# Kernel tuning notes

Hardware: AMD Instinct MI355X
Metric: run time of the kernel (lower is better)

Reference implementation:

```python
import jax, jax.numpy as jnp
import numpy as np

# priors from init_kwargs
PRIOR_PI = 0.5
PRIOR_S1 = 1.0
PRIOR_S2 = 0.0025
LOG_SQRT_2PI = 0.5 * np.log(2.0 * np.pi).astype(np.float32)


def _normal_logprob(x, sigma):
    # Normal(0, sigma).log_prob(x)
    return -0.5 * (x / sigma) ** 2 - jnp.log(sigma) - LOG_SQRT_2PI


def _mixture_logprob_sum(x, pi, sigma1, sigma2):
    # log(pi * N(x;0,s1) + (1-pi) * N(x;0,s2)).sum(), as in the torch code
    p1 = jnp.exp(_normal_logprob(x, sigma1))
    p2 = jnp.exp(_normal_logprob(x, sigma2))
    return jnp.log(pi * p1 + (1.0 - pi) * p2).sum()


def _sample(pi, rho1, rho2, eps, gum):
    # ScaleMixtureGaussian_VarPost.sample(): gumbel-max over (pi, 1-pi)
    sigma1 = jnp.log1p(jnp.exp(rho1))
    sigma2 = jnp.log1p(jnp.exp(rho2))
    x = jnp.stack((pi, 1.0 - pi), axis=-1)          # [..., 2]
    mode = jnp.argmax(x + gum, axis=-1).astype(pi.dtype)  # [...]
    return mode * sigma1 * eps + (1.0 - mode) * sigma2 * eps


def setup_inputs() -> dict:
    key = jax.random.key(0)
    ks = jax.random.split(key, 12)
    OUT, IN, B = 8192, 4096, 128
    f32 = jnp.float32
    u_w = jax.random.uniform(ks[0], (OUT, IN, 2), dtype=f32, minval=1e-6, maxval=1.0 - 1e-6)
    u_b = jax.random.uniform(ks[1], (OUT, 2), dtype=f32, minval=1e-6, maxval=1.0 - 1e-6)
    return {
        "x": jax.random.normal(ks[2], (B, IN), dtype=f32),
        "w_pi": jax.random.uniform(ks[3], (OUT, IN), dtype=f32),
        "w_rho1": 0.1 * jax.random.normal(ks[4], (OUT, IN), dtype=f32),
        "w_rho2": 0.1 * jax.random.normal(ks[5], (OUT, IN), dtype=f32),
        "b_pi": jax.random.uniform(ks[6], (OUT,), dtype=f32),
        "b_rho1": 0.1 * jax.random.normal(ks[7], (OUT,), dtype=f32),
        "b_rho2": 0.1 * jax.random.normal(ks[8], (OUT,), dtype=f32),
        "eps_w": jax.random.normal(ks[9], (OUT, IN), dtype=f32),
        "eps_b": jax.random.normal(ks[10], (OUT,), dtype=f32),
        "gum_w": -jnp.log(-jnp.log(u_w)),  # Gumbel(0,1)
        "gum_b": -jnp.log(-jnp.log(u_b)),
    }


def reference(x, w_pi, w_rho1, w_rho2, b_pi, b_rho1, b_rho2, eps_w, eps_b, gum_w, gum_b):
    weight = _sample(w_pi, w_rho1, w_rho2, eps_w, gum_w)   # [OUT, IN]
    bias = _sample(b_pi, b_rho1, b_rho2, eps_b, gum_b)     # [OUT]

    log_prior = (_mixture_logprob_sum(weight, PRIOR_PI, PRIOR_S1, PRIOR_S2)
                 + _mixture_logprob_sum(bias, PRIOR_PI, PRIOR_S1, PRIOR_S2))

    sig_w1 = jnp.log1p(jnp.exp(w_rho1))
    sig_w2 = jnp.log1p(jnp.exp(w_rho2))
    sig_b1 = jnp.log1p(jnp.exp(b_rho1))
    sig_b2 = jnp.log1p(jnp.exp(b_rho2))
    log_post = (_mixture_logprob_sum(weight, w_pi, sig_w1, sig_w2)
                + _mixture_logprob_sum(bias, b_pi, sig_b1, sig_b2))

    out = x @ weight.T + bias  # F.linear
    return out, log_prior, log_post
```

## Files before the change

kernel.cpp:

```cpp
#include <hip/hip_runtime.h>

#define OUTN 8192
#define INN  4096
#define BN   128

namespace {

typedef __attribute__((ext_vector_type(8))) short bf16x8;
typedef __attribute__((ext_vector_type(4))) float f32x4;

struct alignas(16) f4 { float v[4]; };
struct alignas(8)  h4 { short v[4]; };

constexpr float C_HLOG2PI = 0.91893853f;
constexpr float C_LN2     = 0.69314718f;

__device__ __forceinline__ short f2bf(float f) {
    unsigned u = __float_as_uint(f);
    u += 0x7fffu + ((u >> 16) & 1u);
    return (short)(u >> 16);
}

__device__ __forceinline__ float prior_lp(float w) {
    float lp1 = -0.5f * w * w - C_HLOG2PI;
    float a   = w * 400.0f;
    float lp2 = -0.5f * a * a + 5.0725261f;
    return __logf(0.5f * __expf(lp1) + 0.5f * __expf(lp2));
}
__device__ __forceinline__ float post_lp(float w, float pi_, float s1, float ls1,
                                         float s2, float ls2) {
    float u1  = __fdividef(w, s1);
    float u2  = __fdividef(w, s2);
    float lq1 = -0.5f * u1 * u1 - ls1 - C_HLOG2PI;
    float lq2 = -0.5f * u2 * u2 - ls2 - C_HLOG2PI;
    return __logf(pi_ * __expf(lq1) + (1.0f - pi_) * __expf(lq2));
}
__device__ __forceinline__ float sample_w(float pi_, float rho1, float rho2, float ep,
                                          float g0, float g1,
                                          float& s1, float& ls1, float& s2, float& ls2) {
    s1  = __logf(1.0f + __expf(rho1));
    s2  = __logf(1.0f + __expf(rho2));
    ls1 = __logf(s1);
    ls2 = __logf(s2);
    bool mode1 = ((1.0f - pi_) + g1) > (pi_ + g0);
    return (mode1 ? s1 : s2) * ep;
}

constexpr int OT = 32;
constexpr int KC = 32;
constexpr int NT = 256;
constexpr int KSTR = 40;

__global__ __launch_bounds__(256)
void xcast(const float* __restrict__ x, short* __restrict__ xb)
{
    const int i = (blockIdx.x * 256 + threadIdx.x) * 8;
    f4 a = *(const f4*)&x[i];
    f4 b = *(const f4*)&x[i + 4];
    h4 o0, o1;
    #pragma unroll
    for (int j = 0; j < 4; ++j) { o0.v[j] = f2bf(a.v[j]); o1.v[j] = f2bf(b.v[j]); }
    *(h4*)&xb[i]     = o0;
    *(h4*)&xb[i + 4] = o1;
}

__global__ __launch_bounds__(NT, 6)
void bayes_main(const short* __restrict__ xb,
                const float* __restrict__ w_pi,
                const float* __restrict__ w_rho1,
                const float* __restrict__ w_rho2,
                const float* __restrict__ eps_w,
                const float* __restrict__ gum_w,
                const float* __restrict__ bias,
                float* __restrict__ out,
                float* __restrict__ pbuf,
                float* __restrict__ partials,
                int NS)
{
    __shared__ alignas(16) short Wt[OT][KSTR];
    __shared__ alignas(16) short Xs[BN][KSTR];
    __shared__ float red[8];

    const int tid   = threadIdx.x;
    const int split = blockIdx.x >> 8;
    const int tile  = blockIdx.x & 255;
    const int o0    = tile * OT;

    const int baseCh = 128 / NS;
    const int remCh  = 128 % NS;
    const int nch    = baseCh + (split < remCh ? 1 : 0);
    const int ch0    = split * baseCh + (split < remCh ? split : remCh);
    const int k0     = ch0 * KC;

    float* outp = (split == 0) ? out : pbuf + (size_t)(split - 1) * ((size_t)BN * OUTN);

    const int c = tid & 7;
    const int r = tid >> 3;

    const size_t wbase = (size_t)(o0 + r) * INN + k0;
    const f4* pi4 = (const f4*)(w_pi   + wbase) + c;
    const f4* r14 = (const f4*)(w_rho1 + wbase) + c;
    const f4* r24 = (const f4*)(w_rho2 + wbase) + c;
    const f4* ep4 = (const f4*)(eps_w  + wbase) + c;
    const f4* gm4 = (const f4*)(gum_w  + 2 * wbase) + 2 * c;

    const int xrr = tid >> 1;
    const int xcc = (tid & 1) * 16;
    const short* xsrc = xb + (size_t)xrr * INN + k0 + xcc;

    f32x4 acc00 = {0.f,0.f,0.f,0.f}, acc01 = {0.f,0.f,0.f,0.f};
    f32x4 acc10 = {0.f,0.f,0.f,0.f}, acc11 = {0.f,0.f,0.f,0.f};
    float priorAcc = 0.0f, postAcc = 0.0f;

    const int wv_  = tid >> 6;
    const int lane = tid & 63;
    const int lrow = lane & 15;
    const int lgo  = (lane >> 4) * 8;

    f4 vpi = pi4[0], vr1 = r14[0], vr2 = r24[0], vep = ep4[0];
    f4 vga = gm4[0], vgb = gm4[1];
    bf16x8 xv0 = *(const bf16x8*)(xsrc);
    bf16x8 xv1 = *(const bf16x8*)(xsrc + 8);

    #pragma unroll 1
    for (int t = 0; t < nch; ++t) {
        h4 wb;
        #pragma unroll
        for (int i = 0; i < 4; ++i) {
            const f4& g = (i < 2) ? vga : vgb;
            float g0 = g.v[(i & 1) * 2], g1 = g.v[(i & 1) * 2 + 1];
            float pi_ = vpi.v[i], ep = vep.v[i];
            float s1  = __logf(1.0f + __expf(vr1.v[i]));
            float s2  = __logf(1.0f + __expf(vr2.v[i]));
            float ls1 = __logf(s1), ls2 = __logf(s2);
            bool  m1  = ((1.0f - pi_) + g1) > (pi_ + g0);
            float sm  = m1 ? s1 : s2;
            float so  = m1 ? s2 : s1;
            float lsm = m1 ? ls1 : ls2;
            float lso = m1 ? ls2 : ls1;
            float wm  = m1 ? pi_ : 1.0f - pi_;
            float w   = sm * ep;
            wb.v[i] = f2bf(w);
            float wsq = w * w;
            float dlp = 5.9914645f - 79999.5f * wsq;
            priorAcc += -0.5f * wsq + __logf(1.0f + __expf(dlp));
            float uo   = __fdividef(w, so);
            float epsq = ep * ep;
            float dlq  = 0.5f * (epsq - uo * uo) + (lsm - lso);
            postAcc += -0.5f * epsq - lsm
                       + __logf(wm + (1.0f - wm) * __expf(dlq));
        }

        __syncthreads();
        *(h4*)&Wt[r][4 * c] = wb;
        *(bf16x8*)&Xs[xrr][xcc]     = xv0;
        *(bf16x8*)&Xs[xrr][xcc + 8] = xv1;
        __syncthreads();

        const int tn = (t + 1 < nch) ? t + 1 : 0;
        vpi = pi4[8*tn]; vr1 = r14[8*tn]; vr2 = r24[8*tn]; vep = ep4[8*tn];
        vga = gm4[16*tn]; vgb = gm4[16*tn + 1];
        xv0 = *(const bf16x8*)(xsrc + 32*tn);
        xv1 = *(const bf16x8*)(xsrc + 32*tn + 8);

        bf16x8 a0 = *(const bf16x8*)&Xs[32 * wv_      + lrow][lgo];
        bf16x8 a1 = *(const bf16x8*)&Xs[32 * wv_ + 16 + lrow][lgo];
        bf16x8 b0 = *(const bf16x8*)&Wt[lrow     ][lgo];
        bf16x8 b1 = *(const bf16x8*)&Wt[16 + lrow][lgo];
        acc00 = __builtin_amdgcn_mfma_f32_16x16x32_bf16(a0, b0, acc00, 0, 0, 0);
        acc01 = __builtin_amdgcn_mfma_f32_16x16x32_bf16(a0, b1, acc01, 0, 0, 0);
        acc10 = __builtin_amdgcn_mfma_f32_16x16x32_bf16(a1, b0, acc10, 0, 0, 0);
        acc11 = __builtin_amdgcn_mfma_f32_16x16x32_bf16(a1, b1, acc11, 0, 0, 0);
    }

    {
        const float ne = (float)(4 * nch);
        priorAcc -= ne * (C_HLOG2PI + C_LN2);
        postAcc  -= ne * C_HLOG2PI;
    }

    {
        const int oc = o0 + lrow;
        const int bb = 32 * wv_ + (lane >> 4) * 4;
        const float bv0 = bias ? bias[oc]      : 0.0f;
        const float bv1 = bias ? bias[oc + 16] : 0.0f;
        #pragma unroll
        for (int j = 0; j < 4; ++j) {
            outp[(size_t)(bb      + j) * OUTN + oc     ] = acc00[j] + bv0;
            outp[(size_t)(bb      + j) * OUTN + oc + 16] = acc01[j] + bv1;
            outp[(size_t)(bb + 16 + j) * OUTN + oc     ] = acc10[j] + bv0;
            outp[(size_t)(bb + 16 + j) * OUTN + oc + 16] = acc11[j] + bv1;
        }
    }

    #pragma unroll
    for (int off = 32; off; off >>= 1) {
        priorAcc += __shfl_down(priorAcc, off);
        postAcc  += __shfl_down(postAcc, off);
    }
    if ((tid & 63) == 0) { red[wv_] = priorAcc; red[4 + wv_] = postAcc; }
    __syncthreads();
    if (tid == 0) {
        partials[2*blockIdx.x    ] = red[0] + red[1] + red[2] + red[3];
        partials[2*blockIdx.x + 1] = red[4] + red[5] + red[6] + red[7];
    }
}

__global__ __launch_bounds__(256)
void bayes_bias(const float* __restrict__ b_pi, const float* __restrict__ b_rho1,
                const float* __restrict__ b_rho2, const float* __restrict__ eps_b,
                const float* __restrict__ gum_b,
                float* __restrict__ bias_vals, float* __restrict__ bpart)
{
    __shared__ float red[8];
    const int tid = threadIdx.x;
    const int o = blockIdx.x * 256 + tid;
    float pi_ = b_pi[o], rho1 = b_rho1[o], rho2 = b_rho2[o], ep = eps_b[o];
    float g0 = gum_b[2*o], g1 = gum_b[2*o + 1];
    float s1, ls1, s2, ls2;
    float w = sample_w(pi_, rho1, rho2, ep, g0, g1, s1, ls1, s2, ls2);
    bias_vals[o] = w;
    float pa = prior_lp(w);
    float qa = post_lp(w, pi_, s1, ls1, s2, ls2);
    #pragma unroll
    for (int off = 32; off; off >>= 1) {
        pa += __shfl_down(pa, off);
        qa += __shfl_down(qa, off);
    }
    const int wave = tid >> 6;
    if ((tid & 63) == 0) { red[wave] = pa; red[4 + wave] = qa; }
    __syncthreads();
    if (tid == 0) {
        bpart[2*blockIdx.x    ] = red[0] + red[1] + red[2] + red[3];
        bpart[2*blockIdx.x + 1] = red[4] + red[5] + red[6] + red[7];
    }
}

__global__ __launch_bounds__(256)
void bayes_reduce(float* __restrict__ out, const float* __restrict__ pbuf,
                  const float* __restrict__ bias, int nsplit)
{
    const size_t i = ((size_t)blockIdx.x * 256 + threadIdx.x) * 4;
    const int o = (int)(i & (OUTN - 1));
    f4 a  = *(const f4*)&out[i];
    f4 bq = *(const f4*)&bias[o];
    #pragma unroll 1
    for (int s = 0; s < nsplit - 1; ++s) {
        f4 p = *(const f4*)&pbuf[(size_t)s * ((size_t)BN * OUTN) + i];
        #pragma unroll
        for (int j = 0; j < 4; ++j) a.v[j] += p.v[j];
    }
    #pragma unroll
    for (int j = 0; j < 4; ++j) a.v[j] += bq.v[j];
    *(f4*)&out[i] = a;
}

__global__ __launch_bounds__(256)
void bayes_final(const float* __restrict__ partials, int cnt,
                 float* __restrict__ out_scalars)
{
    __shared__ double sp[4], sq[4];
    const int tid = threadIdx.x;
    double p = 0.0, q = 0.0;
    for (int j = tid; j < cnt; j += 256) {
        p += (double)partials[2*j];
        q += (double)partials[2*j + 1];
    }
    #pragma unroll
    for (int off = 32; off; off >>= 1) {
        p += __shfl_down(p, off);
        q += __shfl_down(q, off);
    }
    const int wave = tid >> 6;
    if ((tid & 63) == 0) { sp[wave] = p; sq[wave] = q; }
    __syncthreads();
    if (tid == 0) {
        out_scalars[0] = (float)(sp[0] + sp[1] + sp[2] + sp[3]);
        out_scalars[1] = (float)(sq[0] + sq[1] + sq[2] + sq[3]);
    }
}

}

extern "C" void kernel_launch(void* const* d_in, const int* in_sizes, int n_in,
                              void* d_out, int out_size, void* d_ws, size_t ws_size,
                              hipStream_t stream) {
    (void)in_sizes; (void)n_in; (void)out_size;
    const float* x      = (const float*)d_in[0];
    const float* w_pi   = (const float*)d_in[1];
    const float* w_rho1 = (const float*)d_in[2];
    const float* w_rho2 = (const float*)d_in[3];
    const float* b_pi   = (const float*)d_in[4];
    const float* b_rho1 = (const float*)d_in[5];
    const float* b_rho2 = (const float*)d_in[6];
    const float* eps_w  = (const float*)d_in[7];
    const float* eps_b  = (const float*)d_in[8];
    const float* gum_w  = (const float*)d_in[9];
    const float* gum_b  = (const float*)d_in[10];

    float* out = (float*)d_out;
    float* ws  = (float*)d_ws;
    float* bias_vals = ws;
    float* partials  = ws + 8192;
    short* xb        = (short*)(ws + 16384);
    float* pbuf      = ws + 540672;

    const size_t outElems = (size_t)BN * OUTN;
    int NS = 1;
    if      (ws_size >= (540672 + 5 * outElems) * sizeof(float)) NS = 6;
    else if (ws_size >= (540672 + 3 * outElems) * sizeof(float)) NS = 4;
    else if (ws_size >= (540672 + 1 * outElems) * sizeof(float)) NS = 2;

    float* bpart = partials + 2 * 256 * NS;
    const int cnt = 256 * NS + 32;

    xcast<<<(BN * INN) / (256 * 8), 256, 0, stream>>>(x, xb);
    bayes_bias<<<32, 256, 0, stream>>>(b_pi, b_rho1, b_rho2, eps_b, gum_b,
                                       bias_vals, bpart);

    if (NS == 1) {
        bayes_main<<<256, NT, 0, stream>>>(xb, w_pi, w_rho1, w_rho2, eps_w, gum_w,
                                           bias_vals, out, pbuf, partials, 1);
    } else {
        bayes_main<<<256 * NS, NT, 0, stream>>>(xb, w_pi, w_rho1, w_rho2, eps_w, gum_w,
                                                nullptr, out, pbuf, partials, NS);
        bayes_reduce<<<(int)(outElems / 4 / 256), 256, 0, stream>>>(out, pbuf,
                                                                    bias_vals, NS);
    }
    bayes_final<<<1, 256, 0, stream>>>(partials, cnt, out + outElems);
}
```

Baseline: 201.5 us.

## Double-buffer LDS tiles in main loop and fuse auxiliary kernels

The main GEMM loop now uses two LDS buffers alternated per chunk, which replaces the two __syncthreads per iteration with a single waitcnt plus barrier. The next chunk's global loads are issued before the barrier. The x-cast and bias-sampling kernels are merged into one prep launch, and the split-K reduction is merged with the final scalar reduction, cutting two kernel launches. The cost is double the LDS per block, which may lower occupancy. The reduction in block 0 depends on every main-kernel partial being written, which stream order guarantees.

Result: slower. 223.6 us (+10.9%).

```diff
diff --git a/kernel.cpp b/kernel.cpp
--- a/kernel.cpp
+++ b/kernel.cpp
@@ -52,16 +52,46 @@
 constexpr int KSTR = 40;
 
 __global__ __launch_bounds__(256)
-void xcast(const float* __restrict__ x, short* __restrict__ xb)
+void prep(const float* __restrict__ x, short* __restrict__ xb,
+          const float* __restrict__ b_pi, const float* __restrict__ b_rho1,
+          const float* __restrict__ b_rho2, const float* __restrict__ eps_b,
+          const float* __restrict__ gum_b,
+          float* __restrict__ bias_vals, float* __restrict__ bpart)
 {
-    const int i = (blockIdx.x * 256 + threadIdx.x) * 8;
-    f4 a = *(const f4*)&x[i];
-    f4 b = *(const f4*)&x[i + 4];
-    h4 o0, o1;
+    __shared__ float red[8];
+    const int tid = threadIdx.x;
+    if (blockIdx.x < 256) {
+        const int i = (blockIdx.x * 256 + tid) * 8;
+        f4 a = *(const f4*)&x[i];
+        f4 b = *(const f4*)&x[i + 4];
+        h4 o0, o1;
+        #pragma unroll
+        for (int j = 0; j < 4; ++j) { o0.v[j] = f2bf(a.v[j]); o1.v[j] = f2bf(b.v[j]); }
+        *(h4*)&xb[i]     = o0;
+        *(h4*)&xb[i + 4] = o1;
+        return;
+    }
+    const int bb = blockIdx.x - 256;
+    const int o = bb * 256 + tid;
+    float pi_ = b_pi[o], rho1 = b_rho1[o], rho2 = b_rho2[o], ep = eps_b[o];
+    float g0 = gum_b[2*o], g1 = gum_b[2*o + 1];
+    float s1, ls1, s2, ls2;
+    float w = sample_w(pi_, rho1, rho2, ep, g0, g1, s1, ls1, s2, ls2);
+    bias_vals[o] = w;
+    float pa = prior_lp(w);
+    float qa = post_lp(w, pi_, s1, ls1, s2, ls2);
     #pragma unroll
-    for (int j = 0; j < 4; ++j) { o0.v[j] = f2bf(a.v[j]); o1.v[j] = f2bf(b.v[j]); }
-    *(h4*)&xb[i]     = o0;
-    *(h4*)&xb[i + 4] = o1;
+    for (int off = 32; off; off >>= 1) {
+        pa += __shfl_down(pa, off);
+        qa += __shfl_down(qa, off);
+    }
+    const int wave = tid >> 6;
+    if ((tid & 63) == 0) { red[wave] = pa; red[4 + wave] = qa; }
+    __syncthreads();
+    if (tid == 0) {
+        bpart[2*bb    ] = red[0] + red[1] + red[2] + red[3];
+        bpart[2*bb + 1] = red[4] + red[5] + red[6] + red[7];
+    }
 }
 
 __global__ __launch_bounds__(NT, 6)
@@ -77,8 +107,8 @@
                 float* __restrict__ partials,
                 int NS)
 {
-    __shared__ alignas(16) short Wt[OT][KSTR];
-    __shared__ alignas(16) short Xs[BN][KSTR];
+    __shared__ alignas(16) short Wt[2][OT][KSTR];
+    __shared__ alignas(16) short Xs[2][BN][KSTR];
     __shared__ float red[8];
 
     const int tid   = threadIdx.x;
@@ -124,6 +154,7 @@
 
     #pragma unroll 1
     for (int t = 0; t < nch; ++t) {
+        const int p = t & 1;
         h4 wb;
         #pragma unroll
         for (int i = 0; i < 4; ++i) {
@@ -151,22 +182,24 @@
                        + __logf(wm + (1.0f - wm) * __expf(dlq));
         }
 
-        __syncthreads();
-        *(h4*)&Wt[r][4 * c] = wb;
-        *(bf16x8*)&Xs[xrr][xcc]     = xv0;
-        *(bf16x8*)&Xs[xrr][xcc + 8] = xv1;
-        __syncthreads();
-
         const int tn = (t + 1 < nch) ? t + 1 : 0;
         vpi = pi4[8*tn]; vr1 = r14[8*tn]; vr2 = r24[8*tn]; vep = ep4[8*tn];
         vga = gm4[16*tn]; vgb = gm4[16*tn + 1];
+
+        *(h4*)&Wt[p][r][4 * c] = wb;
+        *(bf16x8*)&Xs[p][xrr][xcc]     = xv0;
+        *(bf16x8*)&Xs[p][xrr][xcc + 8] = xv1;
         xv0 = *(const bf16x8*)(xsrc + 32*tn);
         xv1 = *(const bf16x8*)(xsrc + 32*tn + 8);
 
-        bf16x8 a0 = *(const bf16x8*)&Xs[32 * wv_      + lrow][lgo];
-        bf16x8 a1 = *(const bf16x8*)&Xs[32 * wv_ + 16 + lrow][lgo];
-        bf16x8 b0 = *(const bf16x8*)&Wt[lrow     ][lgo];
-        bf16x8 b1 = *(const bf16x8*)&Wt[16 + lrow][lgo];
+        asm volatile("s_waitcnt lgkmcnt(0)" ::: "memory");
+        __builtin_amdgcn_s_barrier();
+        asm volatile("" ::: "memory");
+
+        bf16x8 a0 = *(const bf16x8*)&Xs[p][32 * wv_      + lrow][lgo];
+        bf16x8 a1 = *(const bf16x8*)&Xs[p][32 * wv_ + 16 + lrow][lgo];
+        bf16x8 b0 = *(const bf16x8*)&Wt[p][lrow     ][lgo];
+        bf16x8 b1 = *(const bf16x8*)&Wt[p][16 + lrow][lgo];
         acc00 = __builtin_amdgcn_mfma_f32_16x16x32_bf16(a0, b0, acc00, 0, 0, 0);
         acc01 = __builtin_amdgcn_mfma_f32_16x16x32_bf16(a0, b1, acc01, 0, 0, 0);
         acc10 = __builtin_amdgcn_mfma_f32_16x16x32_bf16(a1, b0, acc10, 0, 0, 0);
@@ -207,40 +240,13 @@
 }
 
 __global__ __launch_bounds__(256)
-void bayes_bias(const float* __restrict__ b_pi, const float* __restrict__ b_rho1,
-                const float* __restrict__ b_rho2, const float* __restrict__ eps_b,
-                const float* __restrict__ gum_b,
-                float* __restrict__ bias_vals, float* __restrict__ bpart)
+void reduce_final(float* __restrict__ out, const float* __restrict__ pbuf,
+                  const float* __restrict__ bias, int nsplit,
+                  const float* __restrict__ partials, int cnt,
+                  float* __restrict__ out_scalars)
 {
-    __shared__ float red[8];
     const int tid = threadIdx.x;
-    const int o = blockIdx.x * 256 + tid;
-    float pi_ = b_pi[o], rho1 = b_rho1[o], rho2 = b_rho2[o], ep = eps_b[o];
-    float g0 = gum_b[2*o], g1 = gum_b[2*o + 1];
-    float s1, ls1, s2, ls2;
-    float w = sample_w(pi_, rho1, rho2, ep, g0, g1, s1, ls1, s2, ls2);
-    bias_vals[o] = w;
-    float pa = prior_lp(w);
-    float qa = post_lp(w, pi_, s1, ls1, s2, ls2);
-    #pragma unroll
-    for (int off = 32; off; off >>= 1) {
-        pa += __shfl_down(pa, off);
-        qa += __shfl_down(qa, off);
-    }
-    const int wave = tid >> 6;
-    if ((tid & 63) == 0) { red[wave] = pa; red[4 + wave] = qa; }
-    __syncthreads();
-    if (tid == 0) {
-        bpart[2*blockIdx.x    ] = red[0] + red[1] + red[2] + red[3];
-        bpart[2*blockIdx.x + 1] = red[4] + red[5] + red[6] + red[7];
-    }
-}
-
-__global__ __launch_bounds__(256)
-void bayes_reduce(float* __restrict__ out, const float* __restrict__ pbuf,
-                  const float* __restrict__ bias, int nsplit)
-{
-    const size_t i = ((size_t)blockIdx.x * 256 + threadIdx.x) * 4;
+    const size_t i = ((size_t)blockIdx.x * 256 + tid) * 4;
     const int o = (int)(i & (OUTN - 1));
     f4 a  = *(const f4*)&out[i];
     f4 bq = *(const f4*)&bias[o];
@@ -253,6 +259,27 @@
     #pragma unroll
     for (int j = 0; j < 4; ++j) a.v[j] += bq.v[j];
     *(f4*)&out[i] = a;
+
+    if (blockIdx.x == 0) {
+        __shared__ double sp[4], sq[4];
+        double p = 0.0, q = 0.0;
+        for (int j = tid; j < cnt; j += 256) {
+            p += (double)partials[2*j];
+            q += (double)partials[2*j + 1];
+        }
+        #pragma unroll
+        for (int off = 32; off; off >>= 1) {
+            p += __shfl_down(p, off);
+            q += __shfl_down(q, off);
+        }
+        const int wave = tid >> 6;
+        if ((tid & 63) == 0) { sp[wave] = p; sq[wave] = q; }
+        __syncthreads();
+        if (tid == 0) {
+            out_scalars[0] = (float)(sp[0] + sp[1] + sp[2] + sp[3]);
+            out_scalars[1] = (float)(sq[0] + sq[1] + sq[2] + sq[3]);
+        }
+    }
 }
 
 __global__ __launch_bounds__(256)
@@ -314,18 +341,17 @@
     float* bpart = partials + 2 * 256 * NS;
     const int cnt = 256 * NS + 32;
 
-    xcast<<<(BN * INN) / (256 * 8), 256, 0, stream>>>(x, xb);
-    bayes_bias<<<32, 256, 0, stream>>>(b_pi, b_rho1, b_rho2, eps_b, gum_b,
-                                       bias_vals, bpart);
+    prep<<<288, 256, 0, stream>>>(x, xb, b_pi, b_rho1, b_rho2, eps_b, gum_b,
+                                  bias_vals, bpart);
 
     if (NS == 1) {
         bayes_main<<<256, NT, 0, stream>>>(xb, w_pi, w_rho1, w_rho2, eps_w, gum_w,
                                            bias_vals, out, pbuf, partials, 1);
+        bayes_final<<<1, 256, 0, stream>>>(partials, cnt, out + outElems);
     } else {
         bayes_main<<<256 * NS, NT, 0, stream>>>(xb, w_pi, w_rho1, w_rho2, eps_w, gum_w,
                                                 nullptr, out, pbuf, partials, NS);
-        bayes_reduce<<<(int)(outElems / 4 / 256), 256, 0, stream>>>(out, pbuf,
-                                                                    bias_vals, NS);
-    }
-    bayes_final<<<1, 256, 0, stream>>>(partials, cnt, out + outElems);
-}
+        reduce_final<<<(int)(outElems / 4 / 256), 256, 0, stream>>>(
+            out, pbuf, bias_vals, NS, partials, cnt, out + outElems);
+    }
+}
```

## Fuse x cast into main kernel and bias sampling into reduce

Applied to the files above, without the earlier changes.

Removes the separate x-to-bf16 cast kernel: the main kernel now loads fp32 x and converts it while staging into shared memory. The bias sampling and the final scalar reduction move into the split-K reduce kernel, which recomputes bias values per element and uses one extra block for the log-prob sums. This cuts the launch count from five to two on the default path, at the cost of doubled x load bytes per chunk and redundant bias recomputation.

After: 225.6 us. 1.12x slower.

```diff
diff --git a/kernel.cpp b/kernel.cpp
--- a/kernel.cpp
+++ b/kernel.cpp
@@ -45,6 +45,13 @@
     bool mode1 = ((1.0f - pi_) + g1) > (pi_ + g0);
     return (mode1 ? s1 : s2) * ep;
 }
+__device__ __forceinline__ float sample_val(float pi_, float r1, float r2, float ep,
+                                            float g0, float g1) {
+    float s1 = __logf(1.0f + __expf(r1));
+    float s2 = __logf(1.0f + __expf(r2));
+    bool  m1 = ((1.0f - pi_) + g1) > (pi_ + g0);
+    return (m1 ? s1 : s2) * ep;
+}
 
 constexpr int OT = 32;
 constexpr int KC = 32;
@@ -52,20 +59,37 @@
 constexpr int KSTR = 40;
 
 __global__ __launch_bounds__(256)
-void xcast(const float* __restrict__ x, short* __restrict__ xb)
+void bias_only(const float* __restrict__ b_pi, const float* __restrict__ b_rho1,
+               const float* __restrict__ b_rho2, const float* __restrict__ eps_b,
+               const float* __restrict__ gum_b,
+               float* __restrict__ bias_vals, float* __restrict__ bpart)
 {
-    const int i = (blockIdx.x * 256 + threadIdx.x) * 8;
-    f4 a = *(const f4*)&x[i];
-    f4 b = *(const f4*)&x[i + 4];
-    h4 o0, o1;
-    #pragma unroll
-    for (int j = 0; j < 4; ++j) { o0.v[j] = f2bf(a.v[j]); o1.v[j] = f2bf(b.v[j]); }
-    *(h4*)&xb[i]     = o0;
-    *(h4*)&xb[i + 4] = o1;
+    __shared__ float red[8];
+    const int tid = threadIdx.x;
+    const int o = blockIdx.x * 256 + tid;
+    float pi_ = b_pi[o], rho1 = b_rho1[o], rho2 = b_rho2[o], ep = eps_b[o];
+    float g0 = gum_b[2*o], g1 = gum_b[2*o + 1];
+    float s1, ls1, s2, ls2;
+    float w = sample_w(pi_, rho1, rho2, ep, g0, g1, s1, ls1, s2, ls2);
+    bias_vals[o] = w;
+    float pa = prior_lp(w);
+    float qa = post_lp(w, pi_, s1, ls1, s2, ls2);
+    #pragma unroll
+    for (int off = 32; off; off >>= 1) {
+        pa += __shfl_down(pa, off);
+        qa += __shfl_down(qa, off);
+    }
+    const int wave = tid >> 6;
+    if ((tid & 63) == 0) { red[wave] = pa; red[4 + wave] = qa; }
+    __syncthreads();
+    if (tid == 0) {
+        bpart[2*blockIdx.x    ] = red[0] + red[1] + red[2] + red[3];
+        bpart[2*blockIdx.x + 1] = red[4] + red[5] + red[6] + red[7];
+    }
 }
 
 __global__ __launch_bounds__(NT, 6)
-void bayes_main(const short* __restrict__ xb,
+void bayes_main(const float* __restrict__ x,
                 const float* __restrict__ w_pi,
                 const float* __restrict__ w_rho1,
                 const float* __restrict__ w_rho2,
@@ -106,7 +130,7 @@
 
     const int xrr = tid >> 1;
     const int xcc = (tid & 1) * 16;
-    const short* xsrc = xb + (size_t)xrr * INN + k0 + xcc;
+    const float* xsrc = x + (size_t)xrr * INN + k0 + xcc;
 
     f32x4 acc00 = {0.f,0.f,0.f,0.f}, acc01 = {0.f,0.f,0.f,0.f};
     f32x4 acc10 = {0.f,0.f,0.f,0.f}, acc11 = {0.f,0.f,0.f,0.f};
@@ -119,8 +143,10 @@
 
     f4 vpi = pi4[0], vr1 = r14[0], vr2 = r24[0], vep = ep4[0];
     f4 vga = gm4[0], vgb = gm4[1];
-    bf16x8 xv0 = *(const bf16x8*)(xsrc);
-    bf16x8 xv1 = *(const bf16x8*)(xsrc + 8);
+    f4 xa0 = *(const f4*)(xsrc);
+    f4 xa1 = *(const f4*)(xsrc + 4);
+    f4 xa2 = *(const f4*)(xsrc + 8);
+    f4 xa3 = *(const f4*)(xsrc + 12);
 
     #pragma unroll 1
     for (int t = 0; t < nch; ++t) {
@@ -153,15 +179,27 @@
 
         __syncthreads();
         *(h4*)&Wt[r][4 * c] = wb;
-        *(bf16x8*)&Xs[xrr][xcc]     = xv0;
-        *(bf16x8*)&Xs[xrr][xcc + 8] = xv1;
+        {
+            bf16x8 xb0, xb1;
+            #pragma unroll
+            for (int j = 0; j < 4; ++j) {
+                xb0[j]     = f2bf(xa0.v[j]);
+                xb0[4 + j] = f2bf(xa1.v[j]);
+                xb1[j]     = f2bf(xa2.v[j]);
+                xb1[4 + j] = f2bf(xa3.v[j]);
+            }
+            *(bf16x8*)&Xs[xrr][xcc]     = xb0;
+            *(bf16x8*)&Xs[xrr][xcc + 8] = xb1;
+        }
         __syncthreads();
 
         const int tn = (t + 1 < nch) ? t + 1 : 0;
         vpi = pi4[8*tn]; vr1 = r14[8*tn]; vr2 = r24[8*tn]; vep = ep4[8*tn];
         vga = gm4[16*tn]; vgb = gm4[16*tn + 1];
-        xv0 = *(const bf16x8*)(xsrc + 32*tn);
-        xv1 = *(const bf16x8*)(xsrc + 32*tn + 8);
+        xa0 = *(const f4*)(xsrc + 32*tn);
+        xa1 = *(const f4*)(xsrc + 32*tn + 4);
+        xa2 = *(const f4*)(xsrc + 32*tn + 8);
+        xa3 = *(const f4*)(xsrc + 32*tn + 12);
 
         bf16x8 a0 = *(const bf16x8*)&Xs[32 * wv_      + lrow][lgo];
         bf16x8 a1 = *(const bf16x8*)&Xs[32 * wv_ + 16 + lrow][lgo];
@@ -207,43 +245,73 @@
 }
 
 __global__ __launch_bounds__(256)
-void bayes_bias(const float* __restrict__ b_pi, const float* __restrict__ b_rho1,
-                const float* __restrict__ b_rho2, const float* __restrict__ eps_b,
-                const float* __restrict__ gum_b,
-                float* __restrict__ bias_vals, float* __restrict__ bpart)
+void reduce_final(float* __restrict__ out, const float* __restrict__ pbuf,
+                  int nsplit, const float* __restrict__ partials, int npart,
+                  const float* __restrict__ b_pi, const float* __restrict__ b_rho1,
+                  const float* __restrict__ b_rho2, const float* __restrict__ eps_b,
+                  const float* __restrict__ gum_b,
+                  float* __restrict__ out_scalars)
 {
-    __shared__ float red[8];
     const int tid = threadIdx.x;
-    const int o = blockIdx.x * 256 + tid;
-    float pi_ = b_pi[o], rho1 = b_rho1[o], rho2 = b_rho2[o], ep = eps_b[o];
-    float g0 = gum_b[2*o], g1 = gum_b[2*o + 1];
-    float s1, ls1, s2, ls2;
-    float w = sample_w(pi_, rho1, rho2, ep, g0, g1, s1, ls1, s2, ls2);
-    bias_vals[o] = w;
-    float pa = prior_lp(w);
-    float qa = post_lp(w, pi_, s1, ls1, s2, ls2);
-    #pragma unroll
-    for (int off = 32; off; off >>= 1) {
-        pa += __shfl_down(pa, off);
-        qa += __shfl_down(qa, off);
-    }
-    const int wave = tid >> 6;
-    if ((tid & 63) == 0) { red[wave] = pa; red[4 + wave] = qa; }
-    __syncthreads();
-    if (tid == 0) {
-        bpart[2*blockIdx.x    ] = red[0] + red[1] + red[2] + red[3];
-        bpart[2*blockIdx.x + 1] = red[4] + red[5] + red[6] + red[7];
-    }
-}
-
-__global__ __launch_bounds__(256)
-void bayes_reduce(float* __restrict__ out, const float* __restrict__ pbuf,
-                  const float* __restrict__ bias, int nsplit)
-{
-    const size_t i = ((size_t)blockIdx.x * 256 + threadIdx.x) * 4;
+
+    if (blockIdx.x == 1024) {
+        __shared__ float red[8];
+        __shared__ double sp[4], sq[4];
+        float pa = 0.0f, qa = 0.0f;
+        for (int o = tid; o < OUTN; o += 256) {
+            float s1, ls1, s2, ls2;
+            float w = sample_w(b_pi[o], b_rho1[o], b_rho2[o], eps_b[o],
+                               gum_b[2*o], gum_b[2*o + 1], s1, ls1, s2, ls2);
+            pa += prior_lp(w);
+            qa += post_lp(w, b_pi[o], s1, ls1, s2, ls2);
+        }
+        #pragma unroll
+        for (int off = 32; off; off >>= 1) {
+            pa += __shfl_down(pa, off);
+            qa += __shfl_down(qa, off);
+        }
+        const int wave = tid >> 6;
+        if ((tid & 63) == 0) { red[wave] = pa; red[4 + wave] = qa; }
+
+        double p = 0.0, q = 0.0;
+        for (int j = tid; j < npart; j += 256) {
+            p += (double)partials[2*j];
+            q += (double)partials[2*j + 1];
+        }
+        #pragma unroll
+        for (int off = 32; off; off >>= 1) {
+            p += __shfl_down(p, off);
+            q += __shfl_down(q, off);
+        }
+        if ((tid & 63) == 0) { sp[wave] = p; sq[wave] = q; }
+        __syncthreads();
+        if (tid == 0) {
+            double bp = (double)(red[0] + red[1] + red[2] + red[3]);
+            double bq = (double)(red[4] + red[5] + red[6] + red[7]);
+            out_scalars[0] = (float)(sp[0] + sp[1] + sp[2] + sp[3] + bp);
+            out_scalars[1] = (float)(sq[0] + sq[1] + sq[2] + sq[3] + bq);
+        }
+        return;
+    }
+
+    const size_t i = ((size_t)blockIdx.x * 256 + tid) * 4;
     const int o = (int)(i & (OUTN - 1));
-    f4 a  = *(const f4*)&out[i];
-    f4 bq = *(const f4*)&bias[o];
+
+    f4 bp = *(const f4*)&b_pi[o];
+    f4 b1 = *(const f4*)&b_rho1[o];
+    f4 b2 = *(const f4*)&b_rho2[o];
+    f4 be = *(const f4*)&eps_b[o];
+    f4 g01 = *(const f4*)&gum_b[2*o];
+    f4 g23 = *(const f4*)&gum_b[2*o + 4];
+    f4 bw;
+    #pragma unroll
+    for (int j = 0; j < 4; ++j) {
+        const f4& g = (j < 2) ? g01 : g23;
+        bw.v[j] = sample_val(bp.v[j], b1.v[j], b2.v[j], be.v[j],
+                             g.v[(j & 1) * 2], g.v[(j & 1) * 2 + 1]);
+    }
+
+    f4 a = *(const f4*)&out[i];
     #pragma unroll 1
     for (int s = 0; s < nsplit - 1; ++s) {
         f4 p = *(const f4*)&pbuf[(size_t)s * ((size_t)BN * OUTN) + i];
@@ -251,7 +319,7 @@
         for (int j = 0; j < 4; ++j) a.v[j] += p.v[j];
     }
     #pragma unroll
-    for (int j = 0; j < 4; ++j) a.v[j] += bq.v[j];
+    for (int j = 0; j < 4; ++j) a.v[j] += bw.v[j];
     *(f4*)&out[i] = a;
 }
 
@@ -302,7 +370,6 @@
     float* ws  = (float*)d_ws;
     float* bias_vals = ws;
     float* partials  = ws + 8192;
-    short* xb        = (short*)(ws + 16384);
     float* pbuf      = ws + 540672;
 
     const size_t outElems = (size_t)BN * OUTN;
@@ -311,21 +378,18 @@
     else if (ws_size >= (540672 + 3 * outElems) * sizeof(float)) NS = 4;
     else if (ws_size >= (540672 + 1 * outElems) * sizeof(float)) NS = 2;
 
-    float* bpart = partials + 2 * 256 * NS;
-    const int cnt = 256 * NS + 32;
-
-    xcast<<<(BN * INN) / (256 * 8), 256, 0, stream>>>(x, xb);
-    bayes_bias<<<32, 256, 0, stream>>>(b_pi, b_rho1, b_rho2, eps_b, gum_b,
-                                       bias_vals, bpart);
-
     if (NS == 1) {
-        bayes_main<<<256, NT, 0, stream>>>(xb, w_pi, w_rho1, w_rho2, eps_w, gum_w,
+        float* bpart = partials + 2 * 256;
+        bias_only<<<32, 256, 0, stream>>>(b_pi, b_rho1, b_rho2, eps_b, gum_b,
+                                          bias_vals, bpart);
+        bayes_main<<<256, NT, 0, stream>>>(x, w_pi, w_rho1, w_rho2, eps_w, gum_w,
                                            bias_vals, out, pbuf, partials, 1);
+        bayes_final<<<1, 256, 0, stream>>>(partials, 256 + 32, out + outElems);
     } else {
-        bayes_main<<<256 * NS, NT, 0, stream>>>(xb, w_pi, w_rho1, w_rho2, eps_w, gum_w,
+        bayes_main<<<256 * NS, NT, 0, stream>>>(x, w_pi, w_rho1, w_rho2, eps_w, gum_w,
                                                 nullptr, out, pbuf, partials, NS);
-        bayes_reduce<<<(int)(outElems / 4 / 256), 256, 0, stream>>>(out, pbuf,
-                                                                    bias_vals, NS);
-    }
-    bayes_final<<<1, 256, 0, stream>>>(partials, cnt, out + outElems);
-}
+        reduce_final<<<(int)(outElems / 4 / 256) + 1, 256, 0, stream>>>(
+            out, pbuf, NS, partials, 256 * NS,
+            b_pi, b_rho1, b_rho2, eps_b, gum_b, out + outElems);
+    }
+}
```
